# Performance work log

Hardware: AMD Instinct MI355X
Metric: run time of the kernel (lower is better)

## Reference

```python
import jax, jax.numpy as jnp
import numpy as np
from jax import lax

B, D, H, STEPS = 16384, 256, 256, 25


def setup_inputs() -> dict:
    key = jax.random.key(0)
    k1, k2, k3, k4 = jax.random.split(key, 4)
    s1 = 1.0 / np.sqrt(D)
    s2 = 1.0 / np.sqrt(H)
    return {
        "z0": jax.random.normal(k1, (B, D), dtype=jnp.float32),
        "t_range": jnp.linspace(0.0, 1.0, STEPS, dtype=jnp.float32),
        "W1": jax.random.normal(k2, (D, H), dtype=jnp.float32) * s1,
        "b1": jnp.zeros((H,), dtype=jnp.float32),
        "wt": jax.random.normal(k3, (H,), dtype=jnp.float32) * 0.1,
        "W2": jax.random.normal(k4, (H, D), dtype=jnp.float32) * s2,
        "b2": jnp.zeros((D,), dtype=jnp.float32),
    }


def reference(z0, t_range, W1, b1, wt, W2, b2):
    # Euler solver: zt <- zt + dt * f(zt, t) for every t in t_range
    # (matches euler_solver: note it steps at ALL 25 grid points, incl. t_end)
    dt = t_range[1] - t_range[0]

    def dynamics(z, t):
        h = jnp.tanh(z @ W1 + b1 + t * wt)  # [B, H]
        return h @ W2 + b2                   # [B, D]

    def step(z, t):
        return z + dt * dynamics(z, t), None

    zT, _ = lax.scan(step, z0, t_range)
    return zT
```

## Files before the change

kernel.cpp:

```cpp
#include <hip/hip_runtime.h>

typedef short bf16x8 __attribute__((ext_vector_type(8)));
typedef float f32x4  __attribute__((ext_vector_type(4)));

#define NSTEP 25
#define MROW  16
#define SROW  264
#define LDSB  (MROW * SROW)

__device__ __forceinline__ unsigned short f2bf(float x) {
    union { float f; unsigned int u; } v; v.f = x;
    unsigned int r = v.u + 0x7FFFu + ((v.u >> 16) & 1u);
    return (unsigned short)(r >> 16);
}

#if __has_builtin(__builtin_amdgcn_cvt_pk_bf16_f32)
typedef __bf16 bfv2 __attribute__((ext_vector_type(2)));
__device__ __forceinline__ unsigned int pk2bf(float a, float b) {
    union { bfv2 v; unsigned int u; } c;
    c.v = __builtin_amdgcn_cvt_pk_bf16_f32(a, b);
    return c.u;
}
#else
__device__ __forceinline__ unsigned int pk2bf(float a, float b) {
    return (unsigned int)f2bf(a) | ((unsigned int)f2bf(b) << 16);
}
#endif

__device__ __forceinline__ float tanh_fast(float x) {
    float e = __expf(2.0f * x);
    return 1.0f - 2.0f * __builtin_amdgcn_rcpf(e + 1.0f);
}

__global__ void prep_all(const float* __restrict__ W1,
                         const float* __restrict__ W2,
                         const float* __restrict__ b2,
                         const float* __restrict__ t_range,
                         unsigned short* __restrict__ Wr,
                         unsigned short* __restrict__ W21r,
                         float* __restrict__ c1)
{
    __shared__ float row[256];
    int b = blockIdx.x;
    if (b < 512) {
        const float* src = (b < 256) ? W1 : W2;
        unsigned short* dst = Wr + ((b < 256) ? 0 : 65536);
        int k = b & 255;
        int n = threadIdx.x;
        int p  = (k & ~31) | ((k & 15) << 1) | ((k >> 4) & 1);
        int kc = p >> 5, q = (p >> 3) & 3, j = p & 7;
        dst[kc * 8192 + n * 32 + q * 8 + j] = f2bf(src[k * 256 + n]);
    } else {
        int i = b - 512, j = threadIdx.x;
        row[j] = (i < 256) ? W2[i * 256 + j] : b2[j];
        __syncthreads();
        float acc = 0.f;
        for (int d = 0; d < 256; ++d)
            acc = fmaf(row[d], W1[d * 256 + j], acc);
        if (i < 256) {
            float dt = t_range[1] - t_range[0];
            int p  = (i & ~31) | ((i & 15) << 1) | ((i >> 4) & 1);
            int kc = p >> 5, q = (p >> 3) & 3, jj = p & 7;
            W21r[kc * 8192 + j * 32 + q * 8 + jj] = f2bf(dt * acc);
        } else {
            c1[j] = acc;
        }
    }
}

__global__ __launch_bounds__(512, 4) void ode_main(
    const float* __restrict__ z0,
    const float* __restrict__ t_range,
    const float* __restrict__ b1,
    const float* __restrict__ wt,
    const float* __restrict__ b2,
    const unsigned short* __restrict__ W1r,
    const unsigned short* __restrict__ W2r,
    const unsigned short* __restrict__ W21r,
    const float* __restrict__ c1,
    float* __restrict__ out)
{
    __shared__ __align__(16) unsigned short As[2 * LDSB];

    const int tid  = threadIdx.x;
    const int wave = tid >> 6;
    const int lane = tid & 63;
    const int q    = lane >> 4;
    const int l15  = lane & 15;
    const int row0 = blockIdx.x * MROW;
    const int n0   = wave * 32;

    const float dt = t_range[1] - t_range[0];

    float bt[2], dbt[2];
#pragma unroll
    for (int tt = 0; tt < 2; ++tt) {
        int n = n0 + tt * 16 + l15;
        bt[tt]  = b1[n];
        dbt[tt] = dt * (wt[n] + c1[n]);
    }

#pragma unroll
    for (int r = 0; r < 4; ++r) {
        int m = q * 4 + r;
        const float* zr = &z0[(row0 + m) * 256 + n0];
        *(unsigned int*)&As[m * SROW + n0 + l15 * 2] =
            pk2bf(zr[l15], zr[16 + l15]);
    }
    __syncthreads();

    f32x4 y[2];
    y[0] = f32x4{0.f, 0.f, 0.f, 0.f};
    y[1] = f32x4{0.f, 0.f, 0.f, 0.f};
#pragma unroll
    for (int kc = 0; kc < 8; ++kc) {
        bf16x8 a = *(const bf16x8*)&As[l15 * SROW + kc * 32 + q * 8];
#pragma unroll
        for (int tt = 0; tt < 2; ++tt) {
            bf16x8 bb = *(const bf16x8*)&W1r[kc * 8192 + (n0 + tt * 16 + l15) * 32 + q * 8];
            y[tt] = __builtin_amdgcn_mfma_f32_16x16x32_bf16(a, bb, y[tt], 0, 0, 0);
        }
    }

    bf16x8 w21f[8][2];
#pragma unroll
    for (int kc = 0; kc < 8; ++kc)
#pragma unroll
        for (int tt = 0; tt < 2; ++tt)
            w21f[kc][tt] = *(const bf16x8*)&W21r[kc * 8192 + (n0 + tt * 16 + l15) * 32 + q * 8];

    f32x4 S[2];
    S[0] = f32x4{0.f, 0.f, 0.f, 0.f};
    S[1] = f32x4{0.f, 0.f, 0.f, 0.f};

    for (int s = 0; s < NSTEP - 1; ++s) {
        const int buf = ((s + 1) & 1) * LDSB;
#pragma unroll
        for (int r = 0; r < 4; ++r) {
            int m = q * 4 + r;
            float h0 = tanh_fast(y[0][r] + bt[0]);
            float h1 = tanh_fast(y[1][r] + bt[1]);
            S[0][r] += h0; S[1][r] += h1;
            *(unsigned int*)&As[buf + m * SROW + n0 + l15 * 2] = pk2bf(h0, h1);
        }
        __syncthreads();

#pragma unroll
        for (int kc = 0; kc < 8; ++kc) {
            bf16x8 a = *(const bf16x8*)&As[buf + l15 * SROW + kc * 32 + q * 8];
            y[0] = __builtin_amdgcn_mfma_f32_16x16x32_bf16(a, w21f[kc][0], y[0], 0, 0, 0);
            y[1] = __builtin_amdgcn_mfma_f32_16x16x32_bf16(a, w21f[kc][1], y[1], 0, 0, 0);
        }

#pragma unroll
        for (int tt = 0; tt < 2; ++tt) bt[tt] += dbt[tt];
    }

#pragma unroll
    for (int r = 0; r < 4; ++r)
#pragma unroll
        for (int tt = 0; tt < 2; ++tt)
            S[tt][r] += tanh_fast(y[tt][r] + bt[tt]);

    {
        const int buf = LDSB;
#pragma unroll
        for (int r = 0; r < 4; ++r) {
            int m = q * 4 + r;
            *(unsigned int*)&As[buf + m * SROW + n0 + l15 * 2] =
                pk2bf(S[0][r], S[1][r]);
        }
        __syncthreads();

        f32x4 acc[2];
        acc[0] = f32x4{0.f, 0.f, 0.f, 0.f};
        acc[1] = f32x4{0.f, 0.f, 0.f, 0.f};
#pragma unroll
        for (int kc = 0; kc < 8; ++kc) {
            bf16x8 a = *(const bf16x8*)&As[buf + l15 * SROW + kc * 32 + q * 8];
#pragma unroll
            for (int tt = 0; tt < 2; ++tt) {
                bf16x8 bb = *(const bf16x8*)&W2r[kc * 8192 + (n0 + tt * 16 + l15) * 32 + q * 8];
                acc[tt] = __builtin_amdgcn_mfma_f32_16x16x32_bf16(a, bb, acc[tt], 0, 0, 0);
            }
        }

        const float cb2 = (float)NSTEP * dt;
#pragma unroll
        for (int tt = 0; tt < 2; ++tt) {
            float b2v = b2[n0 + tt * 16 + l15];
#pragma unroll
            for (int r = 0; r < 4; ++r) {
                int idx = (row0 + q * 4 + r) * 256 + n0 + tt * 16 + l15;
                out[idx] = z0[idx] + dt * acc[tt][r] + cb2 * b2v;
            }
        }
    }
}

extern "C" void kernel_launch(void* const* d_in, const int* in_sizes, int n_in,
                              void* d_out, int out_size, void* d_ws, size_t ws_size,
                              hipStream_t stream) {
    const float* z0      = (const float*)d_in[0];
    const float* t_range = (const float*)d_in[1];
    const float* W1      = (const float*)d_in[2];
    const float* b1      = (const float*)d_in[3];
    const float* wt      = (const float*)d_in[4];
    const float* W2      = (const float*)d_in[5];
    const float* b2      = (const float*)d_in[6];

    unsigned short* Wr = (unsigned short*)d_ws;
    unsigned short* W1r  = Wr;
    unsigned short* W2r  = Wr + 65536;
    unsigned short* W21r = Wr + 131072;
    float*          c1   = (float*)(Wr + 196608);

    prep_all<<<769, 256, 0, stream>>>(W1, W2, b2, t_range, Wr, W21r, c1);
    ode_main<<<1024, 512, 0, stream>>>(z0, t_range, b1, wt, b2,
                                       W1r, W2r, W21r, c1, (float*)d_out);
}
```

Baseline: 155.7 us.

## Split each block's output columns across 16 waves and unroll prep reduction

The main kernel now launches 1024 threads per block, so each wave owns one 16-column tile instead of two. This halves per-wave register state (the W21 fragments and accumulators) and doubles the waves available to hide MFMA and tanh latency. It also writes h as scattered single bf16 stores into a permuted LDS position instead of packed pairs. The prep kernel's dot-product loop is split into four independent accumulators to break the FMA dependency chain. The trade-off is more LDS store instructions per step and a heavier barrier across 16 waves per block.

New measurement: 163.0 us. 4.7% more time.

```diff
diff --git a/kernel.cpp b/kernel.cpp
--- a/kernel.cpp
+++ b/kernel.cpp
@@ -54,9 +54,14 @@
         int i = b - 512, j = threadIdx.x;
         row[j] = (i < 256) ? W2[i * 256 + j] : b2[j];
         __syncthreads();
-        float acc = 0.f;
-        for (int d = 0; d < 256; ++d)
-            acc = fmaf(row[d], W1[d * 256 + j], acc);
+        float a0 = 0.f, a1 = 0.f, a2 = 0.f, a3 = 0.f;
+        for (int d = 0; d < 256; d += 4) {
+            a0 = fmaf(row[d    ], W1[(d    ) * 256 + j], a0);
+            a1 = fmaf(row[d + 1], W1[(d + 1) * 256 + j], a1);
+            a2 = fmaf(row[d + 2], W1[(d + 2) * 256 + j], a2);
+            a3 = fmaf(row[d + 3], W1[(d + 3) * 256 + j], a3);
+        }
+        float acc = (a0 + a1) + (a2 + a3);
         if (i < 256) {
             float dt = t_range[1] - t_range[0];
             int p  = (i & ~31) | ((i & 15) << 1) | ((i >> 4) & 1);
@@ -68,7 +73,7 @@
     }
 }
 
-__global__ __launch_bounds__(512, 4) void ode_main(
+__global__ __launch_bounds__(1024, 8) void ode_main(
     const float* __restrict__ z0,
     const float* __restrict__ t_range,
     const float* __restrict__ b1,
@@ -88,112 +93,87 @@
     const int q    = lane >> 4;
     const int l15  = lane & 15;
     const int row0 = blockIdx.x * MROW;
-    const int n0   = wave * 32;
+    const int n    = wave * 16 + l15;
+    const int pos  = ((n >> 5) << 5) + ((n & 15) << 1) + ((n >> 4) & 1);
 
     const float dt = t_range[1] - t_range[0];
-
-    float bt[2], dbt[2];
-#pragma unroll
-    for (int tt = 0; tt < 2; ++tt) {
-        int n = n0 + tt * 16 + l15;
-        bt[tt]  = b1[n];
-        dbt[tt] = dt * (wt[n] + c1[n]);
-    }
-
-#pragma unroll
-    for (int r = 0; r < 4; ++r) {
-        int m = q * 4 + r;
-        const float* zr = &z0[(row0 + m) * 256 + n0];
-        *(unsigned int*)&As[m * SROW + n0 + l15 * 2] =
-            pk2bf(zr[l15], zr[16 + l15]);
+    float bt  = b1[n];
+    float dbt = dt * (wt[n] + c1[n]);
+
+    {
+        int pp = tid & 127;
+        int c0 = ((pp >> 4) << 5) + (pp & 15);
+#pragma unroll
+        for (int it = 0; it < 2; ++it) {
+            int m = (tid >> 7) + it * 8;
+            const float* zr = &z0[(row0 + m) * 256];
+            *(unsigned int*)&As[m * SROW + (pp << 1)] = pk2bf(zr[c0], zr[c0 + 16]);
+        }
     }
     __syncthreads();
 
-    f32x4 y[2];
-    y[0] = f32x4{0.f, 0.f, 0.f, 0.f};
-    y[1] = f32x4{0.f, 0.f, 0.f, 0.f};
+    f32x4 y = f32x4{0.f, 0.f, 0.f, 0.f};
 #pragma unroll
     for (int kc = 0; kc < 8; ++kc) {
-        bf16x8 a = *(const bf16x8*)&As[l15 * SROW + kc * 32 + q * 8];
-#pragma unroll
-        for (int tt = 0; tt < 2; ++tt) {
-            bf16x8 bb = *(const bf16x8*)&W1r[kc * 8192 + (n0 + tt * 16 + l15) * 32 + q * 8];
-            y[tt] = __builtin_amdgcn_mfma_f32_16x16x32_bf16(a, bb, y[tt], 0, 0, 0);
-        }
-    }
-
-    bf16x8 w21f[8][2];
+        bf16x8 a  = *(const bf16x8*)&As[l15 * SROW + kc * 32 + q * 8];
+        bf16x8 bb = *(const bf16x8*)&W1r[kc * 8192 + n * 32 + q * 8];
+        y = __builtin_amdgcn_mfma_f32_16x16x32_bf16(a, bb, y, 0, 0, 0);
+    }
+
+    bf16x8 w21f[8];
 #pragma unroll
     for (int kc = 0; kc < 8; ++kc)
-#pragma unroll
-        for (int tt = 0; tt < 2; ++tt)
-            w21f[kc][tt] = *(const bf16x8*)&W21r[kc * 8192 + (n0 + tt * 16 + l15) * 32 + q * 8];
-
-    f32x4 S[2];
-    S[0] = f32x4{0.f, 0.f, 0.f, 0.f};
-    S[1] = f32x4{0.f, 0.f, 0.f, 0.f};
-
+        w21f[kc] = *(const bf16x8*)&W21r[kc * 8192 + n * 32 + q * 8];
+
+    f32x4 S = f32x4{0.f, 0.f, 0.f, 0.f};
+
+#pragma unroll 2
     for (int s = 0; s < NSTEP - 1; ++s) {
         const int buf = ((s + 1) & 1) * LDSB;
 #pragma unroll
         for (int r = 0; r < 4; ++r) {
             int m = q * 4 + r;
-            float h0 = tanh_fast(y[0][r] + bt[0]);
-            float h1 = tanh_fast(y[1][r] + bt[1]);
-            S[0][r] += h0; S[1][r] += h1;
-            *(unsigned int*)&As[buf + m * SROW + n0 + l15 * 2] = pk2bf(h0, h1);
+            float h = tanh_fast(y[r] + bt);
+            S[r] += h;
+            As[buf + m * SROW + pos] = f2bf(h);
         }
         __syncthreads();
 
 #pragma unroll
         for (int kc = 0; kc < 8; ++kc) {
             bf16x8 a = *(const bf16x8*)&As[buf + l15 * SROW + kc * 32 + q * 8];
-            y[0] = __builtin_amdgcn_mfma_f32_16x16x32_bf16(a, w21f[kc][0], y[0], 0, 0, 0);
-            y[1] = __builtin_amdgcn_mfma_f32_16x16x32_bf16(a, w21f[kc][1], y[1], 0, 0, 0);
-        }
-
-#pragma unroll
-        for (int tt = 0; tt < 2; ++tt) bt[tt] += dbt[tt];
+            y = __builtin_amdgcn_mfma_f32_16x16x32_bf16(a, w21f[kc], y, 0, 0, 0);
+        }
+        bt += dbt;
     }
 
 #pragma unroll
     for (int r = 0; r < 4; ++r)
-#pragma unroll
-        for (int tt = 0; tt < 2; ++tt)
-            S[tt][r] += tanh_fast(y[tt][r] + bt[tt]);
+        S[r] += tanh_fast(y[r] + bt);
 
     {
         const int buf = LDSB;
 #pragma unroll
         for (int r = 0; r < 4; ++r) {
             int m = q * 4 + r;
-            *(unsigned int*)&As[buf + m * SROW + n0 + l15 * 2] =
-                pk2bf(S[0][r], S[1][r]);
+            As[buf + m * SROW + pos] = f2bf(S[r]);
         }
         __syncthreads();
 
-        f32x4 acc[2];
-        acc[0] = f32x4{0.f, 0.f, 0.f, 0.f};
-        acc[1] = f32x4{0.f, 0.f, 0.f, 0.f};
+        f32x4 acc = f32x4{0.f, 0.f, 0.f, 0.f};
 #pragma unroll
         for (int kc = 0; kc < 8; ++kc) {
-            bf16x8 a = *(const bf16x8*)&As[buf + l15 * SROW + kc * 32 + q * 8];
-#pragma unroll
-            for (int tt = 0; tt < 2; ++tt) {
-                bf16x8 bb = *(const bf16x8*)&W2r[kc * 8192 + (n0 + tt * 16 + l15) * 32 + q * 8];
-                acc[tt] = __builtin_amdgcn_mfma_f32_16x16x32_bf16(a, bb, acc[tt], 0, 0, 0);
-            }
+            bf16x8 a  = *(const bf16x8*)&As[buf + l15 * SROW + kc * 32 + q * 8];
+            bf16x8 bb = *(const bf16x8*)&W2r[kc * 8192 + n * 32 + q * 8];
+            acc = __builtin_amdgcn_mfma_f32_16x16x32_bf16(a, bb, acc, 0, 0, 0);
         }
 
         const float cb2 = (float)NSTEP * dt;
-#pragma unroll
-        for (int tt = 0; tt < 2; ++tt) {
-            float b2v = b2[n0 + tt * 16 + l15];
-#pragma unroll
-            for (int r = 0; r < 4; ++r) {
-                int idx = (row0 + q * 4 + r) * 256 + n0 + tt * 16 + l15;
-                out[idx] = z0[idx] + dt * acc[tt][r] + cb2 * b2v;
-            }
+        const float b2v = b2[n];
+#pragma unroll
+        for (int r = 0; r < 4; ++r) {
+            int idx = (row0 + q * 4 + r) * 256 + n;
+            out[idx] = z0[idx] + dt * acc[r] + cb2 * b2v;
         }
     }
 }
@@ -216,6 +196,6 @@
     float*          c1   = (float*)(Wr + 196608);
 
     prep_all<<<769, 256, 0, stream>>>(W1, W2, b2, t_range, Wr, W21r, c1);
-    ode_main<<<1024, 512, 0, stream>>>(z0, t_range, b1, wt, b2,
-                                       W1r, W2r, W21r, c1, (float*)d_out);
-}
+    ode_main<<<1024, 1024, 0, stream>>>(z0, t_range, b1, wt, b2,
+                                        W1r, W2r, W21r, c1, (float*)d_out);
+}
```
